# Kernel optimization log

Hardware: AMD Instinct MI355X
Metric: run time of the kernel (lower is better)

## Reference

```python
import jax, jax.numpy as jnp
import numpy as np

EPS, GAMMA, LAMB, C1, C2 = 0.2, 0.99, 0.95, 0.5, 0.01
T = 8388608  # 2**23 timesteps


def setup_inputs() -> dict:
    key = jax.random.key(0)
    k1, k2, k3, k4 = jax.random.split(key, 4)
    # probs in (0.1, 1.0) to keep ratios / log well-conditioned
    probs = jax.random.uniform(k1, (T,), jnp.float32, 0.1, 1.0)
    probs_old = jax.random.uniform(k2, (T,), jnp.float32, 0.1, 1.0)
    rewards = jax.random.normal(k3, (T,), jnp.float32)
    values = jax.random.normal(k4, (T,), jnp.float32)
    return {"probs": probs, "probs_old": probs_old,
            "rewards": rewards, "values": values}


def _calc_gaes(rewards, values):
    # delta_t = r_t - v_t + gamma * v_{t+1}, with v_T = 0
    v_next = jnp.concatenate([values[1:], jnp.zeros((1,), values.dtype)])
    delta = rewards - values + GAMMA * v_next
    def step(gae, d):
        gae = GAMMA * LAMB * gae + d
        return gae, gae
    _, gaes = jax.lax.scan(step, jnp.float32(0.0), delta, reverse=True)
    return gaes


def _calc_value_targets(rewards):
    def step(acc, r):
        acc = acc * GAMMA + r
        return acc, acc
    _, targets = jax.lax.scan(step, jnp.float32(0.0), rewards, reverse=True)
    return targets


def reference(probs, probs_old, rewards, values):
    advantages = _calc_gaes(rewards, values)
    ratio = probs / probs_old
    clipped = jnp.clip(ratio, 1.0 - EPS, 1.0 + EPS)
    clip_loss = -jnp.sum(jnp.minimum(ratio * advantages, clipped * advantages))
    values_target = _calc_value_targets(rewards)
    value_loss = jnp.sum((values - values_target) ** 2)  # MSELoss(sum)
    entropy_loss = -jnp.sum(probs * jnp.log(probs + 1e-5))
    return clip_loss + C1 * value_loss + C2 * entropy_loss
```

## Files before the change

### kernel.cpp

```cpp
#include <hip/hip_runtime.h>


#define T_TOTAL 8388608L
#define CHUNK   2048
#define NBLK    4096
#define NT      256
#define NW      4

#define EPSF 0.2f
#define GF   0.99f
#define C1F  0.5f
#define C2F  0.01f
#define AGLF ((float)(0.99 * 0.95))

constexpr float fpowc(double a, int n) {
    double r = 1.0;
    for (int i = 0; i < n; ++i) r *= a;
    return (float)r;
}
constexpr float AG4   = fpowc(0.99 * 0.95, 4);
constexpr float AG8   = fpowc(0.99 * 0.95, 8);
constexpr float AG16  = fpowc(0.99 * 0.95, 16);
constexpr float AG32  = fpowc(0.99 * 0.95, 32);
constexpr float AG64  = fpowc(0.99 * 0.95, 64);
constexpr float AG128 = fpowc(0.99 * 0.95, 128);
constexpr float AG256 = fpowc(0.99 * 0.95, 256);
constexpr float AG512 = fpowc(0.99 * 0.95, 512);
constexpr float G4    = fpowc(0.99, 4);
constexpr float G8    = fpowc(0.99, 8);
constexpr float G16   = fpowc(0.99, 16);
constexpr float G32   = fpowc(0.99, 32);
constexpr float G64   = fpowc(0.99, 64);
constexpr float G128  = fpowc(0.99, 128);
constexpr float G256  = fpowc(0.99, 256);
constexpr float G512  = fpowc(0.99, 512);

__device__ __forceinline__ float wscan(float val, float w, int lane) {
#pragma unroll
    for (int s = 1; s < 64; s <<= 1) {
        float o = __shfl_down(val, s, 64);
        val += (lane + s < 64) ? w * o : 0.0f;
        w *= w;
    }
    return val;
}

__device__ __forceinline__ float g8(const float4& a, const float4& b, int i) {
    const float4 f = (i < 4) ? a : b;
    const int k = i & 3;
    return k == 0 ? f.x : k == 1 ? f.y : k == 2 ? f.z : f.w;
}

__global__ __launch_bounds__(NT) void ppo_main(
    const float* __restrict__ probs,
    const float* __restrict__ probs_old,
    const float* __restrict__ rewards,
    const float* __restrict__ values,
    float* __restrict__ out)
{
    __shared__ float sx[16];
    __shared__ float sRed[NW];

    const int  j    = threadIdx.x;
    const int  lane = j & 63;
    const int  wid  = j >> 6;
    const int  c    = blockIdx.x;
    const long base = (long)c * CHUNK;
    const long g0   = base + 8L * j;
    const bool has_halo = (c != NBLK - 1);

    const float4 r40 = *reinterpret_cast<const float4*>(rewards + g0);
    const float4 r41 = *reinterpret_cast<const float4*>(rewards + g0 + 4);
    const float4 v40 = *reinterpret_cast<const float4*>(values  + g0);
    const float4 v41 = *reinterpret_cast<const float4*>(values  + g0 + 4);
    const long we = base + 512L * (wid + 1);
    const float vwend = (we < T_TOTAL) ? values[we] : 0.0f;

    float4 hr4 = make_float4(0,0,0,0), hv4 = make_float4(0,0,0,0);
    float  hvn = 0.0f;
    if (has_halo) {
        const long hb = base + CHUNK + 4L * j;
        hr4 = *reinterpret_cast<const float4*>(rewards + hb);
        hv4 = *reinterpret_cast<const float4*>(values  + hb);
        hvn = values[base + CHUNK + 256L * wid + 256];
    }
    const float4 p40 = *reinterpret_cast<const float4*>(probs     + g0);
    const float4 p41 = *reinterpret_cast<const float4*>(probs     + g0 + 4);
    const float4 q40 = *reinterpret_cast<const float4*>(probs_old + g0);
    const float4 q41 = *reinterpret_cast<const float4*>(probs_old + g0 + 4);

    float vn7;
    {
        float t = __shfl_down(v40.x, 1, 64);
        vn7 = (lane < 63) ? t : vwend;
    }
    float d[8];
#pragma unroll
    for (int i = 0; i < 7; ++i) d[i] = g8(r40, r41, i) - g8(v40, v41, i) + GF * g8(v40, v41, i + 1);
    d[7] = r41.w - v41.w + GF * vn7;

    float Pg = 0.0f, Pr = 0.0f;
#pragma unroll
    for (int i = 7; i >= 0; --i) {
        Pg = fmaf(AGLF, Pg, d[i]);
        Pr = fmaf(GF,   Pr, g8(r40, r41, i));
    }
    const float Ug = wscan(Pg, AG8, lane);
    const float Ur = wscan(Pr, G8,  lane);
    float sng = __shfl_down(Ug, 1, 64); sng = (lane < 63) ? sng : 0.0f;
    float snr = __shfl_down(Ur, 1, 64); snr = (lane < 63) ? snr : 0.0f;

    float hg = 0.0f, hr = 0.0f;
    {
        float t = __shfl_down(hv4.x, 1, 64);
        const float vn3 = (lane < 63) ? t : hvn;
        const float d0 = hr4.x - hv4.x + GF * hv4.y;
        const float d1 = hr4.y - hv4.y + GF * hv4.z;
        const float d2 = hr4.z - hv4.z + GF * hv4.w;
        const float d3 = hr4.w - hv4.w + GF * vn3;
        float pwg = 1.f, pwr = 1.f;
        if (lane & 1)  { pwg *= AG4;   pwr *= G4;   }
        if (lane & 2)  { pwg *= AG8;   pwr *= G8;   }
        if (lane & 4)  { pwg *= AG16;  pwr *= G16;  }
        if (lane & 8)  { pwg *= AG32;  pwr *= G32;  }
        if (lane & 16) { pwg *= AG64;  pwr *= G64;  }
        if (lane & 32) { pwg *= AG128; pwr *= G128; }
        hg = (d0 + AGLF * (d1 + AGLF * (d2 + AGLF * d3))) * pwg;
        hr = (hr4.x + GF * (hr4.y + GF * (hr4.z + GF * hr4.w))) * pwr;
#pragma unroll
        for (int t2 = 1; t2 < 64; t2 <<= 1) {
            hg += __shfl_xor(hg, t2, 64);
            hr += __shfl_xor(hr, t2, 64);
        }
    }
    if (lane == 0) {
        sx[wid]      = hg;
        sx[4 + wid]  = hr;
        sx[8 + wid]  = Ug;
        sx[12 + wid] = Ur;
    }

    float rt[8];
    float acc = 0.0f;
#pragma unroll
    for (int i = 0; i < 8; ++i) {
        const float pi = g8(p40, p41, i);
        rt[i] = __fdividef(pi, g8(q40, q41, i));
        acc -= C2F * pi * __logf(pi + 1e-5f);
    }

    __builtin_amdgcn_sched_barrier(0);
    asm volatile("s_waitcnt lgkmcnt(0)" ::: "memory");
    __builtin_amdgcn_s_barrier();
    __builtin_amdgcn_sched_barrier(0);

    const float4 Hgv = *reinterpret_cast<const float4*>(&sx[0]);
    const float4 Hrv = *reinterpret_cast<const float4*>(&sx[4]);
    const float4 Wgv = *reinterpret_cast<const float4*>(&sx[8]);
    const float4 Wrv = *reinterpret_cast<const float4*>(&sx[12]);

    float Kg = Hgv.x + AG256 * (Hgv.y + AG256 * (Hgv.z + AG256 * Hgv.w));
    float Kr = Hrv.x + G256  * (Hrv.y + G256  * (Hrv.z + G256  * Hrv.w));
    float Cg = Kg, Cr = Kr;
    if (3 > wid) { Cg = fmaf(AG512, Cg, Wgv.w); Cr = fmaf(G512, Cr, Wrv.w); }
    if (2 > wid) { Cg = fmaf(AG512, Cg, Wgv.z); Cr = fmaf(G512, Cr, Wrv.z); }
    if (1 > wid) { Cg = fmaf(AG512, Cg, Wgv.y); Cr = fmaf(G512, Cr, Wrv.y); }

    const int k63 = 63 - lane;
    float wgl = 1.f, wrl = 1.f;
    if (k63 & 1)  { wgl *= AG8;   wrl *= G8;   }
    if (k63 & 2)  { wgl *= AG16;  wrl *= G16;  }
    if (k63 & 4)  { wgl *= AG32;  wrl *= G32;  }
    if (k63 & 8)  { wgl *= AG64;  wrl *= G64;  }
    if (k63 & 16) { wgl *= AG128; wrl *= G128; }
    if (k63 & 32) { wgl *= AG256; wrl *= G256; }

    float y  = fmaf(wgl, Cg, sng);
    float tt = fmaf(wrl, Cr, snr);

#pragma unroll
    for (int i = 7; i >= 0; --i) {
        y  = fmaf(AGLF, y, d[i]);
        tt = fmaf(GF, tt, g8(r40, r41, i));
        const float rti  = rt[i];
        const float cl   = fminf(fmaxf(rti, 1.0f - EPSF), 1.0f + EPSF);
        const float term = fminf(rti * y, cl * y);
        const float vd   = g8(v40, v41, i) - tt;
        acc = fmaf(C1F * vd, vd, acc) - term;
    }

#pragma unroll
    for (int t = 32; t >= 1; t >>= 1) acc += __shfl_down(acc, t, 64);
    if (lane == 0) sRed[wid] = acc;
    __syncthreads();
    if (j == 0) atomicAdd(out, (sRed[0] + sRed[1]) + (sRed[2] + sRed[3]));
}

extern "C" void kernel_launch(void* const* d_in, const int* in_sizes, int n_in,
                              void* d_out, int out_size, void* d_ws, size_t ws_size,
                              hipStream_t stream) {
    const float* probs     = (const float*)d_in[0];
    const float* probs_old = (const float*)d_in[1];
    const float* rewards   = (const float*)d_in[2];
    const float* values    = (const float*)d_in[3];
    float* out = (float*)d_out;

    hipMemsetAsync(out, 0, sizeof(float), stream);
    ppo_main<<<NBLK, NT, 0, stream>>>(probs, probs_old, rewards, values, out);
}
```

Before: 173.3 us.

## Grow per-thread work to 32 elements and pipeline prob loads through the loss loop

Quadruples the chunk per block (fewer blocks, 32 timesteps per thread), so the fixed 1024-element look-ahead halo for the reverse scans is read less often relative to useful data. This cuts redundant reward and value traffic. Scan decay constants are extended to match the new spacing. probs and probs_old loads are double-buffered in float4 blocks and interleaved with the backward loss loop. The cost is more registers per thread, possibly lower occupancy, and strided per-lane loads.

```diff
diff --git a/kernel.cpp b/kernel.cpp
--- a/kernel.cpp
+++ b/kernel.cpp
@@ -2,10 +2,11 @@
 
 
 #define T_TOTAL 8388608L
-#define CHUNK   2048
-#define NBLK    4096
+#define CHUNK   8192
+#define NBLK    1024
 #define NT      256
 #define NW      4
+#define MPT     32
 
 #define EPSF 0.2f
 #define GF   0.99f
@@ -16,24 +17,28 @@
 constexpr float fpowc(double a, int n) {
     double r = 1.0;
     for (int i = 0; i < n; ++i) r *= a;
-    return (float)r;
-}
-constexpr float AG4   = fpowc(0.99 * 0.95, 4);
-constexpr float AG8   = fpowc(0.99 * 0.95, 8);
-constexpr float AG16  = fpowc(0.99 * 0.95, 16);
-constexpr float AG32  = fpowc(0.99 * 0.95, 32);
-constexpr float AG64  = fpowc(0.99 * 0.95, 64);
-constexpr float AG128 = fpowc(0.99 * 0.95, 128);
-constexpr float AG256 = fpowc(0.99 * 0.95, 256);
-constexpr float AG512 = fpowc(0.99 * 0.95, 512);
-constexpr float G4    = fpowc(0.99, 4);
-constexpr float G8    = fpowc(0.99, 8);
-constexpr float G16   = fpowc(0.99, 16);
-constexpr float G32   = fpowc(0.99, 32);
-constexpr float G64   = fpowc(0.99, 64);
-constexpr float G128  = fpowc(0.99, 128);
-constexpr float G256  = fpowc(0.99, 256);
-constexpr float G512  = fpowc(0.99, 512);
+    return (r < 1e-40) ? 0.0f : (float)r;
+}
+constexpr float AG4    = fpowc(0.99 * 0.95, 4);
+constexpr float AG8    = fpowc(0.99 * 0.95, 8);
+constexpr float AG16   = fpowc(0.99 * 0.95, 16);
+constexpr float AG32   = fpowc(0.99 * 0.95, 32);
+constexpr float AG64   = fpowc(0.99 * 0.95, 64);
+constexpr float AG128  = fpowc(0.99 * 0.95, 128);
+constexpr float AG256  = fpowc(0.99 * 0.95, 256);
+constexpr float AG512  = fpowc(0.99 * 0.95, 512);
+constexpr float AG1024 = fpowc(0.99 * 0.95, 1024);
+constexpr float AG2048 = fpowc(0.99 * 0.95, 2048);
+constexpr float G4     = fpowc(0.99, 4);
+constexpr float G8     = fpowc(0.99, 8);
+constexpr float G16    = fpowc(0.99, 16);
+constexpr float G32    = fpowc(0.99, 32);
+constexpr float G64    = fpowc(0.99, 64);
+constexpr float G128   = fpowc(0.99, 128);
+constexpr float G256   = fpowc(0.99, 256);
+constexpr float G512   = fpowc(0.99, 512);
+constexpr float G1024  = fpowc(0.99, 1024);
+constexpr float G2048  = fpowc(0.99, 2048);
 
 __device__ __forceinline__ float wscan(float val, float w, int lane) {
 #pragma unroll
@@ -45,10 +50,32 @@
     return val;
 }
 
-__device__ __forceinline__ float g8(const float4& a, const float4& b, int i) {
-    const float4 f = (i < 4) ? a : b;
+__device__ __forceinline__ float gx(const float4* a, int i) {
+    const float4 f = a[i >> 2];
     const int k = i & 3;
     return k == 0 ? f.x : k == 1 ? f.y : k == 2 ? f.z : f.w;
+}
+
+__device__ __forceinline__ void lossblk(
+    int bb, const float4& PP, const float4& QQ,
+    const float4* r4, const float4* v4, float vlast,
+    float& y, float& tt, float& acc)
+{
+    const float pp[4] = { PP.x, PP.y, PP.z, PP.w };
+    const float qq[4] = { QQ.x, QQ.y, QQ.z, QQ.w };
+#pragma unroll
+    for (int k = 3; k >= 0; --k) {
+        const int i = 4 * bb + k;
+        const float vn = (i < MPT - 1) ? gx(v4, i + 1) : vlast;
+        const float dd = gx(r4, i) - gx(v4, i) + GF * vn;
+        y  = fmaf(AGLF, y, dd);
+        tt = fmaf(GF, tt, gx(r4, i));
+        const float rt   = __fdividef(pp[k], qq[k]);
+        const float cl   = fminf(fmaxf(rt, 1.0f - EPSF), 1.0f + EPSF);
+        const float term = fminf(rt * y, cl * y);
+        const float vd   = gx(v4, i) - tt;
+        acc = fmaf(C1F * vd, vd, acc) - term - C2F * pp[k] * __logf(pp[k] + 1e-5f);
+    }
 }
 
 __global__ __launch_bounds__(NT) void ppo_main(
@@ -58,7 +85,7 @@
     const float* __restrict__ values,
     float* __restrict__ out)
 {
-    __shared__ float sx[16];
+    __shared__ __align__(16) float sx[16];
     __shared__ float sRed[NW];
 
     const int  j    = threadIdx.x;
@@ -66,15 +93,16 @@
     const int  wid  = j >> 6;
     const int  c    = blockIdx.x;
     const long base = (long)c * CHUNK;
-    const long g0   = base + 8L * j;
+    const long g0   = base + (long)MPT * j;
     const bool has_halo = (c != NBLK - 1);
 
-    const float4 r40 = *reinterpret_cast<const float4*>(rewards + g0);
-    const float4 r41 = *reinterpret_cast<const float4*>(rewards + g0 + 4);
-    const float4 v40 = *reinterpret_cast<const float4*>(values  + g0);
-    const float4 v41 = *reinterpret_cast<const float4*>(values  + g0 + 4);
-    const long we = base + 512L * (wid + 1);
-    const float vwend = (we < T_TOTAL) ? values[we] : 0.0f;
+    float4 r4[8], v4[8];
+#pragma unroll
+    for (int b = 0; b < 8; ++b) {
+        r4[b] = *reinterpret_cast<const float4*>(rewards + g0 + 4 * b);
+        v4[b] = *reinterpret_cast<const float4*>(values  + g0 + 4 * b);
+    }
+    const float vlast = (g0 + MPT < T_TOTAL) ? values[g0 + MPT] : 0.0f;
 
     float4 hr4 = make_float4(0,0,0,0), hv4 = make_float4(0,0,0,0);
     float  hvn = 0.0f;
@@ -84,29 +112,17 @@
         hv4 = *reinterpret_cast<const float4*>(values  + hb);
         hvn = values[base + CHUNK + 256L * wid + 256];
     }
-    const float4 p40 = *reinterpret_cast<const float4*>(probs     + g0);
-    const float4 p41 = *reinterpret_cast<const float4*>(probs     + g0 + 4);
-    const float4 q40 = *reinterpret_cast<const float4*>(probs_old + g0);
-    const float4 q41 = *reinterpret_cast<const float4*>(probs_old + g0 + 4);
-
-    float vn7;
-    {
-        float t = __shfl_down(v40.x, 1, 64);
-        vn7 = (lane < 63) ? t : vwend;
-    }
-    float d[8];
-#pragma unroll
-    for (int i = 0; i < 7; ++i) d[i] = g8(r40, r41, i) - g8(v40, v41, i) + GF * g8(v40, v41, i + 1);
-    d[7] = r41.w - v41.w + GF * vn7;
 
     float Pg = 0.0f, Pr = 0.0f;
 #pragma unroll
-    for (int i = 7; i >= 0; --i) {
-        Pg = fmaf(AGLF, Pg, d[i]);
-        Pr = fmaf(GF,   Pr, g8(r40, r41, i));
-    }
-    const float Ug = wscan(Pg, AG8, lane);
-    const float Ur = wscan(Pr, G8,  lane);
+    for (int i = MPT - 1; i >= 0; --i) {
+        const float vn = (i < MPT - 1) ? gx(v4, i + 1) : vlast;
+        const float dd = gx(r4, i) - gx(v4, i) + GF * vn;
+        Pg = fmaf(AGLF, Pg, dd);
+        Pr = fmaf(GF,   Pr, gx(r4, i));
+    }
+    const float Ug = wscan(Pg, AG32, lane);
+    const float Ur = wscan(Pr, G32,  lane);
     float sng = __shfl_down(Ug, 1, 64); sng = (lane < 63) ? sng : 0.0f;
     float snr = __shfl_down(Ur, 1, 64); snr = (lane < 63) ? snr : 0.0f;
 
@@ -140,14 +156,10 @@
         sx[12 + wid] = Ur;
     }
 
-    float rt[8];
-    float acc = 0.0f;
-#pragma unroll
-    for (int i = 0; i < 8; ++i) {
-        const float pi = g8(p40, p41, i);
-        rt[i] = __fdividef(pi, g8(q40, q41, i));
-        acc -= C2F * pi * __logf(pi + 1e-5f);
-    }
+    float4 pA = *reinterpret_cast<const float4*>(probs     + g0 + 28);
+    float4 qA = *reinterpret_cast<const float4*>(probs_old + g0 + 28);
+    float4 pB = *reinterpret_cast<const float4*>(probs     + g0 + 24);
+    float4 qB = *reinterpret_cast<const float4*>(probs_old + g0 + 24);
 
     __builtin_amdgcn_sched_barrier(0);
     asm volatile("s_waitcnt lgkmcnt(0)" ::: "memory");
@@ -162,32 +174,43 @@
     float Kg = Hgv.x + AG256 * (Hgv.y + AG256 * (Hgv.z + AG256 * Hgv.w));
     float Kr = Hrv.x + G256  * (Hrv.y + G256  * (Hrv.z + G256  * Hrv.w));
     float Cg = Kg, Cr = Kr;
-    if (3 > wid) { Cg = fmaf(AG512, Cg, Wgv.w); Cr = fmaf(G512, Cr, Wrv.w); }
-    if (2 > wid) { Cg = fmaf(AG512, Cg, Wgv.z); Cr = fmaf(G512, Cr, Wrv.z); }
-    if (1 > wid) { Cg = fmaf(AG512, Cg, Wgv.y); Cr = fmaf(G512, Cr, Wrv.y); }
+    if (3 > wid) { Cg = fmaf(AG2048, Cg, Wgv.w); Cr = fmaf(G2048, Cr, Wrv.w); }
+    if (2 > wid) { Cg = fmaf(AG2048, Cg, Wgv.z); Cr = fmaf(G2048, Cr, Wrv.z); }
+    if (1 > wid) { Cg = fmaf(AG2048, Cg, Wgv.y); Cr = fmaf(G2048, Cr, Wrv.y); }
 
     const int k63 = 63 - lane;
     float wgl = 1.f, wrl = 1.f;
-    if (k63 & 1)  { wgl *= AG8;   wrl *= G8;   }
-    if (k63 & 2)  { wgl *= AG16;  wrl *= G16;  }
-    if (k63 & 4)  { wgl *= AG32;  wrl *= G32;  }
-    if (k63 & 8)  { wgl *= AG64;  wrl *= G64;  }
-    if (k63 & 16) { wgl *= AG128; wrl *= G128; }
-    if (k63 & 32) { wgl *= AG256; wrl *= G256; }
+    if (k63 & 1)  { wgl *= AG32;   wrl *= G32;   }
+    if (k63 & 2)  { wgl *= AG64;   wrl *= G64;   }
+    if (k63 & 4)  { wgl *= AG128;  wrl *= G128;  }
+    if (k63 & 8)  { wgl *= AG256;  wrl *= G256;  }
+    if (k63 & 16) { wgl *= AG512;  wrl *= G512;  }
+    if (k63 & 32) { wgl *= AG1024; wrl *= G1024; }
 
     float y  = fmaf(wgl, Cg, sng);
     float tt = fmaf(wrl, Cr, snr);
 
-#pragma unroll
-    for (int i = 7; i >= 0; --i) {
-        y  = fmaf(AGLF, y, d[i]);
-        tt = fmaf(GF, tt, g8(r40, r41, i));
-        const float rti  = rt[i];
-        const float cl   = fminf(fmaxf(rti, 1.0f - EPSF), 1.0f + EPSF);
-        const float term = fminf(rti * y, cl * y);
-        const float vd   = g8(v40, v41, i) - tt;
-        acc = fmaf(C1F * vd, vd, acc) - term;
-    }
+    float acc = 0.0f;
+    lossblk(7, pA, qA, r4, v4, vlast, y, tt, acc);
+    pA = *reinterpret_cast<const float4*>(probs     + g0 + 20);
+    qA = *reinterpret_cast<const float4*>(probs_old + g0 + 20);
+    lossblk(6, pB, qB, r4, v4, vlast, y, tt, acc);
+    pB = *reinterpret_cast<const float4*>(probs     + g0 + 16);
+    qB = *reinterpret_cast<const float4*>(probs_old + g0 + 16);
+    lossblk(5, pA, qA, r4, v4, vlast, y, tt, acc);
+    pA = *reinterpret_cast<const float4*>(probs     + g0 + 12);
+    qA = *reinterpret_cast<const float4*>(probs_old + g0 + 12);
+    lossblk(4, pB, qB, r4, v4, vlast, y, tt, acc);
+    pB = *reinterpret_cast<const float4*>(probs     + g0 + 8);
+    qB = *reinterpret_cast<const float4*>(probs_old + g0 + 8);
+    lossblk(3, pA, qA, r4, v4, vlast, y, tt, acc);
+    pA = *reinterpret_cast<const float4*>(probs     + g0 + 4);
+    qA = *reinterpret_cast<const float4*>(probs_old + g0 + 4);
+    lossblk(2, pB, qB, r4, v4, vlast, y, tt, acc);
+    pB = *reinterpret_cast<const float4*>(probs     + g0);
+    qB = *reinterpret_cast<const float4*>(probs_old + g0);
+    lossblk(1, pA, qA, r4, v4, vlast, y, tt, acc);
+    lossblk(0, pB, qB, r4, v4, vlast, y, tt, acc);
 
 #pragma unroll
     for (int t = 32; t >= 1; t >>= 1) acc += __shfl_down(acc, t, 64);
```

Result: faster. 158.9 us (-8.3%).
